# Kernel optimization log

Measured on AMD Instinct MI355X. Metric: run time of the kernel, lower is better.

The kernel has to match this reference:

```python
import jax, jax.numpy as jnp
import numpy as np

N = 50000

def _norm_coeffs(edge_index, n):
    # add self-loops, compute symmetric GCN normalization D^-1/2 (A+I) D^-1/2
    loops = jnp.arange(n, dtype=edge_index.dtype)
    src = jnp.concatenate([edge_index[0], loops])
    dst = jnp.concatenate([edge_index[1], loops])
    deg = jax.ops.segment_sum(jnp.ones_like(dst, dtype=jnp.float32), dst, num_segments=n)
    dinv = jnp.where(deg > 0, jax.lax.rsqrt(deg), 0.0)
    norm = dinv[src] * dinv[dst]  # [E+N]
    return src, dst, norm

def _gcn(x, W, b, src, dst, norm, n):
    h = x @ W                                   # [N, out]
    m = h[src] * norm[:, None]                  # [E+N, out] gather + scale
    return jax.ops.segment_sum(m, dst, num_segments=n) + b

def setup_inputs() -> dict:
    key = jax.random.key(0)
    ks = jax.random.split(key, 8)
    d, h = 96, 96
    E = 800000
    return {
        "x": jax.random.normal(ks[0], (N, d), jnp.float32),
        "edge_index": jax.random.randint(ks[1], (2, E), 0, N, dtype=jnp.int64),
        "h_prev": jax.random.normal(ks[2], (N, h), jnp.float32),
        "Wx": jax.random.normal(ks[3], (d, h), jnp.float32) * (1.0 / np.sqrt(d)),
        "bx": jnp.zeros((h,), jnp.float32),
        "Wuh": jax.random.normal(ks[4], (2 * h, h), jnp.float32) * (1.0 / np.sqrt(2 * h)),
        "buh": jnp.zeros((h,), jnp.float32),
        "Wch": jax.random.normal(ks[5], (2 * h, h), jnp.float32) * (1.0 / np.sqrt(2 * h)),
        "bch": jnp.zeros((h,), jnp.float32),
    }

def reference(x, edge_index, h_prev, Wx, bx, Wuh, buh, Wch, bch):
    n = x.shape[0]
    src, dst, norm = _norm_coeffs(edge_index, n)
    x_gcn = _gcn(x, Wx, bx, src, dst, norm, n)
    combined = jnp.concatenate([x_gcn, h_prev], axis=1)
    # original computes gcn_uh(combined) twice for u and r; identical math -> compute once
    g = jax.nn.sigmoid(_gcn(combined, Wuh, buh, src, dst, norm, n))
    u = g
    r = g
    combined_r = jnp.concatenate([x_gcn, r * h_prev], axis=1)
    c = jnp.tanh(_gcn(combined_r, Wch, bch, src, dst, norm, n))
    return u * h_prev + (1.0 - u) * c
```

## Files before the change

### kernel.cpp

```cpp
#include <hip/hip_runtime.h>
#include <hip/hip_bf16.h>

#define D 96
typedef long long i64;

typedef __bf16 bf16x8 __attribute__((ext_vector_type(8)));
typedef float f32x16 __attribute__((ext_vector_type(16)));

__device__ __forceinline__ float bf2f(unsigned short u) {
  union { unsigned u; float f; } x; x.u = ((unsigned)u) << 16; return x.f;
}
__device__ __forceinline__ void unpack8(uint4 p, float* a) {
  a[0] = bf2f((unsigned short)(p.x & 0xffff)); a[1] = bf2f((unsigned short)(p.x >> 16));
  a[2] = bf2f((unsigned short)(p.y & 0xffff)); a[3] = bf2f((unsigned short)(p.y >> 16));
  a[4] = bf2f((unsigned short)(p.z & 0xffff)); a[5] = bf2f((unsigned short)(p.z >> 16));
  a[6] = bf2f((unsigned short)(p.w & 0xffff)); a[7] = bf2f((unsigned short)(p.w >> 16));
}

__global__ __launch_bounds__(256) void k_zero_detect(int* deg, int N,
                                                     const unsigned* __restrict__ w,
                                                     int* flag, int E) {
  int i = blockIdx.x * 256 + threadIdx.x;
  if (i < N) deg[i] = 0;
  if (blockIdx.x == 0 && threadIdx.x < 64) {
    int lane = threadIdx.x;
    int lim = (E < 2048) ? E : 2048;
    unsigned acc = 0;
    for (int j = lane; j < lim; j += 64) acc |= w[2 * j + 1];
#pragma unroll
    for (int off = 32; off > 0; off >>= 1) acc |= __shfl_down(acc, off, 64);
    if (lane == 0) *flag = (acc == 0) ? 1 : 0;
  }
}

__global__ __launch_bounds__(256) void k_fillpad(const int* __restrict__ e32,
                                                 const i64* __restrict__ e64,
                                                 const int* __restrict__ flagp,
                                                 int* deg, int* __restrict__ csrp,
                                                 int E, int N) {
  int f = *flagp;
  int stride = gridDim.x * 256;
  for (int i = blockIdx.x * 256 + threadIdx.x; i < E; i += stride) {
    int d = f ? (int)e64[(size_t)E + i] : e32[(size_t)E + i];
    if ((unsigned)d >= (unsigned)N) continue;
    int s = f ? (int)e64[i] : e32[i];
    int r = atomicAdd(&deg[d], 1);
    if (r < 128) csrp[((size_t)d << 7) + r] = s;
  }
}

template <int KTOT, int MODE>
__global__ __launch_bounds__(256) void gemm_mfma(
    const float* __restrict__ xin, const float* __restrict__ xg,
    const float* __restrict__ hprev, const float* __restrict__ gmul,
    const float* __restrict__ W, const int* __restrict__ deg,
    __hip_bfloat16* __restrict__ t, int N) {
  __shared__ __align__(16) unsigned short Ah[4][129][8];
  __shared__ __align__(16) unsigned short Al[4][129][8];
  __shared__ __align__(16) unsigned short Wh[4][97][8];
  __shared__ __align__(16) unsigned short Wl[4][97][8];
  const int tid = threadIdx.x;
  const int lane = tid & 63;
  const int wave = tid >> 6;
  const int lr = lane & 31;
  const int kg = lane >> 5;
  const int rb = blockIdx.x * 128;

  f32x16 acc0, acc1, acc2;
#pragma unroll
  for (int i = 0; i < 16; i++) { acc0[i] = 0.f; acc1[i] = 0.f; acc2[i] = 0.f; }

  const int arow = tid >> 3;
  const int ak0 = (tid & 7) * 4;

  for (int kc = 0; kc < KTOT; kc += 32) {
    if (kc) __syncthreads();
#pragma unroll
    for (int p = 0; p < 4; p++) {
      int row = arow + p * 32;
      int grow = rb + row;
      float4 v = make_float4(0.f, 0.f, 0.f, 0.f);
      int gk = kc + ak0;
      if (grow < N) {
        if (MODE == 0) {
          v = *(const float4*)&xin[(size_t)grow * D + gk];
        } else if (gk < 96) {
          v = *(const float4*)&xg[(size_t)grow * D + gk];
        } else {
          v = *(const float4*)&hprev[(size_t)grow * D + (gk - 96)];
          if (MODE == 2) {
            float4 gm = *(const float4*)&gmul[(size_t)grow * D + (gk - 96)];
            v.x *= gm.x; v.y *= gm.y; v.z *= gm.z; v.w *= gm.w;
          }
        }
      }
      unsigned ux = __float_as_uint(v.x), uy = __float_as_uint(v.y);
      unsigned uz = __float_as_uint(v.z), uw = __float_as_uint(v.w);
      unsigned h01 = (uy & 0xffff0000u) | (ux >> 16);
      unsigned h23 = (uw & 0xffff0000u) | (uz >> 16);
      float lx = v.x - __uint_as_float(ux & 0xffff0000u);
      float ly = v.y - __uint_as_float(uy & 0xffff0000u);
      float lz = v.z - __uint_as_float(uz & 0xffff0000u);
      float lw = v.w - __uint_as_float(uw & 0xffff0000u);
      unsigned l01 = (__float_as_uint(ly) & 0xffff0000u) | (__float_as_uint(lx) >> 16);
      unsigned l23 = (__float_as_uint(lw) & 0xffff0000u) | (__float_as_uint(lz) >> 16);
      int kb = ak0 >> 3, ki = ak0 & 7;
      *(uint2*)&Ah[kb][row][ki] = make_uint2(h01, h23);
      *(uint2*)&Al[kb][row][ki] = make_uint2(l01, l23);
    }
#pragma unroll
    for (int p = 0; p < 3; p++) {
      int idx = tid + p * 256;
      int kq = idx / 96;
      int c = idx - kq * 96;
      int k0 = kq * 4;
      const float* wp = &W[(size_t)(kc + k0) * D + c];
      float w0 = wp[0], w1 = wp[D], w2 = wp[2 * D], w3 = wp[3 * D];
      unsigned u0 = __float_as_uint(w0), u1 = __float_as_uint(w1);
      unsigned u2 = __float_as_uint(w2), u3 = __float_as_uint(w3);
      unsigned h01 = (u1 & 0xffff0000u) | (u0 >> 16);
      unsigned h23 = (u3 & 0xffff0000u) | (u2 >> 16);
      float l0 = w0 - __uint_as_float(u0 & 0xffff0000u);
      float l1 = w1 - __uint_as_float(u1 & 0xffff0000u);
      float l2 = w2 - __uint_as_float(u2 & 0xffff0000u);
      float l3 = w3 - __uint_as_float(u3 & 0xffff0000u);
      unsigned l01 = (__float_as_uint(l1) & 0xffff0000u) | (__float_as_uint(l0) >> 16);
      unsigned l23 = (__float_as_uint(l3) & 0xffff0000u) | (__float_as_uint(l2) >> 16);
      int kb = k0 >> 3, ki = k0 & 7;
      *(uint2*)&Wh[kb][c][ki] = make_uint2(h01, h23);
      *(uint2*)&Wl[kb][c][ki] = make_uint2(l01, l23);
    }
    __syncthreads();
#pragma unroll
    for (int s = 0; s < 2; s++) {
      int kb = 2 * s + kg;
      bf16x8 ah = *(const bf16x8*)&Ah[kb][32 * wave + lr][0];
      bf16x8 al = *(const bf16x8*)&Al[kb][32 * wave + lr][0];
      bf16x8 b0h = *(const bf16x8*)&Wh[kb][lr][0];
      bf16x8 b1h = *(const bf16x8*)&Wh[kb][32 + lr][0];
      bf16x8 b2h = *(const bf16x8*)&Wh[kb][64 + lr][0];
      bf16x8 b0l = *(const bf16x8*)&Wl[kb][lr][0];
      bf16x8 b1l = *(const bf16x8*)&Wl[kb][32 + lr][0];
      bf16x8 b2l = *(const bf16x8*)&Wl[kb][64 + lr][0];
      acc0 = __builtin_amdgcn_mfma_f32_32x32x16_bf16(ah, b0h, acc0, 0, 0, 0);
      acc1 = __builtin_amdgcn_mfma_f32_32x32x16_bf16(ah, b1h, acc1, 0, 0, 0);
      acc2 = __builtin_amdgcn_mfma_f32_32x32x16_bf16(ah, b2h, acc2, 0, 0, 0);
      acc0 = __builtin_amdgcn_mfma_f32_32x32x16_bf16(al, b0h, acc0, 0, 0, 0);
      acc1 = __builtin_amdgcn_mfma_f32_32x32x16_bf16(al, b1h, acc1, 0, 0, 0);
      acc2 = __builtin_amdgcn_mfma_f32_32x32x16_bf16(al, b2h, acc2, 0, 0, 0);
      acc0 = __builtin_amdgcn_mfma_f32_32x32x16_bf16(ah, b0l, acc0, 0, 0, 0);
      acc1 = __builtin_amdgcn_mfma_f32_32x32x16_bf16(ah, b1l, acc1, 0, 0, 0);
      acc2 = __builtin_amdgcn_mfma_f32_32x32x16_bf16(ah, b2l, acc2, 0, 0, 0);
    }
  }
  const int rbase = rb + 32 * wave + 4 * kg;
#pragma unroll
  for (int r = 0; r < 16; r++) {
    int row = rbase + (r & 3) + 8 * (r >> 2);
    if (row >= N) continue;
    float dv = rsqrtf((float)deg[row] + 1.0f);
    __hip_bfloat16* tp = &t[(size_t)row * D];
    tp[lr]      = __float2bfloat16(acc0[r] * dv);
    tp[lr + 32] = __float2bfloat16(acc1[r] * dv);
    tp[lr + 64] = __float2bfloat16(acc2[r] * dv);
  }
}

template <int MODE>
__global__ __launch_bounds__(256) void gather_fin(
    const __hip_bfloat16* __restrict__ t, const int* __restrict__ deg,
    const int* __restrict__ csrp,
    const float* __restrict__ bias,
    const float* __restrict__ g, const float* __restrict__ hprev,
    float* __restrict__ outf, int N) {
  int idx = blockIdx.x * 256 + threadIdx.x;
  int total = N * 12;
  if (idx >= total) return;
  int v = idx / 12;
  int c8 = idx - v * 12;
  const uint4* t8 = (const uint4*)t;
  float acc[8];
  unpack8(t8[(size_t)v * 12 + c8], acc);
  int dv_i = deg[v];
  int b0 = v << 7;
  int b1 = b0 + min(dv_i, 128);
  int j = b0;
  for (; j + 8 <= b1; j += 8) {
    int s0 = csrp[j],     s1 = csrp[j + 1], s2 = csrp[j + 2], s3 = csrp[j + 3];
    int s4 = csrp[j + 4], s5 = csrp[j + 5], s6 = csrp[j + 6], s7 = csrp[j + 7];
    uint4 p0 = t8[(size_t)s0 * 12 + c8];
    uint4 p1 = t8[(size_t)s1 * 12 + c8];
    uint4 p2 = t8[(size_t)s2 * 12 + c8];
    uint4 p3 = t8[(size_t)s3 * 12 + c8];
    uint4 p4 = t8[(size_t)s4 * 12 + c8];
    uint4 p5 = t8[(size_t)s5 * 12 + c8];
    uint4 p6 = t8[(size_t)s6 * 12 + c8];
    uint4 p7 = t8[(size_t)s7 * 12 + c8];
    float a0[8], a1[8], a2[8], a3[8], a4[8], a5[8], a6[8], a7[8];
    unpack8(p0, a0); unpack8(p1, a1); unpack8(p2, a2); unpack8(p3, a3);
    unpack8(p4, a4); unpack8(p5, a5); unpack8(p6, a6); unpack8(p7, a7);
#pragma unroll
    for (int q = 0; q < 8; q++)
      acc[q] += ((a0[q] + a1[q]) + (a2[q] + a3[q])) + ((a4[q] + a5[q]) + (a6[q] + a7[q]));
  }
  for (; j + 4 <= b1; j += 4) {
    int s0 = csrp[j], s1 = csrp[j + 1], s2 = csrp[j + 2], s3 = csrp[j + 3];
    uint4 p0 = t8[(size_t)s0 * 12 + c8];
    uint4 p1 = t8[(size_t)s1 * 12 + c8];
    uint4 p2 = t8[(size_t)s2 * 12 + c8];
    uint4 p3 = t8[(size_t)s3 * 12 + c8];
    float a0[8], a1[8], a2[8], a3[8];
    unpack8(p0, a0); unpack8(p1, a1); unpack8(p2, a2); unpack8(p3, a3);
#pragma unroll
    for (int q = 0; q < 8; q++) acc[q] += (a0[q] + a1[q]) + (a2[q] + a3[q]);
  }
  for (; j < b1; j++) {
    int s = csrp[j];
    float a0[8];
    unpack8(t8[(size_t)s * 12 + c8], a0);
#pragma unroll
    for (int q = 0; q < 8; q++) acc[q] += a0[q];
  }
  float dv = rsqrtf((float)dv_i + 1.0f);
  float4 bA = ((const float4*)bias)[c8 * 2];
  float4 bB = ((const float4*)bias)[c8 * 2 + 1];
  float z[8] = {dv * acc[0] + bA.x, dv * acc[1] + bA.y, dv * acc[2] + bA.z, dv * acc[3] + bA.w,
                dv * acc[4] + bB.x, dv * acc[5] + bB.y, dv * acc[6] + bB.z, dv * acc[7] + bB.w};
  float4 oA, oB;
  if (MODE == 1) {
    oA = make_float4(z[0], z[1], z[2], z[3]);
    oB = make_float4(z[4], z[5], z[6], z[7]);
  } else if (MODE == 2) {
    oA = make_float4(1.0f / (1.0f + expf(-z[0])), 1.0f / (1.0f + expf(-z[1])),
                     1.0f / (1.0f + expf(-z[2])), 1.0f / (1.0f + expf(-z[3])));
    oB = make_float4(1.0f / (1.0f + expf(-z[4])), 1.0f / (1.0f + expf(-z[5])),
                     1.0f / (1.0f + expf(-z[6])), 1.0f / (1.0f + expf(-z[7])));
  } else {
    float4 uA = ((const float4*)g)[idx * 2], uB = ((const float4*)g)[idx * 2 + 1];
    float4 hA = ((const float4*)hprev)[idx * 2], hB = ((const float4*)hprev)[idx * 2 + 1];
    oA = make_float4(uA.x * hA.x + (1.0f - uA.x) * tanhf(z[0]),
                     uA.y * hA.y + (1.0f - uA.y) * tanhf(z[1]),
                     uA.z * hA.z + (1.0f - uA.z) * tanhf(z[2]),
                     uA.w * hA.w + (1.0f - uA.w) * tanhf(z[3]));
    oB = make_float4(uB.x * hB.x + (1.0f - uB.x) * tanhf(z[4]),
                     uB.y * hB.y + (1.0f - uB.y) * tanhf(z[5]),
                     uB.z * hB.z + (1.0f - uB.z) * tanhf(z[6]),
                     uB.w * hB.w + (1.0f - uB.w) * tanhf(z[7]));
  }
  ((float4*)outf)[idx * 2] = oA;
  ((float4*)outf)[idx * 2 + 1] = oB;
}

extern "C" void kernel_launch(void* const* d_in, const int* in_sizes, int n_in,
                              void* d_out, int out_size, void* d_ws, size_t ws_size,
                              hipStream_t stream) {
  const float* x = (const float*)d_in[0];
  const int* ei32 = (const int*)d_in[1];
  const i64* ei64 = (const i64*)d_in[1];
  const unsigned* eiw = (const unsigned*)d_in[1];
  const float* hp = (const float*)d_in[2];
  const float* Wx = (const float*)d_in[3];
  const float* bx = (const float*)d_in[4];
  const float* Wuh = (const float*)d_in[5];
  const float* buh = (const float*)d_in[6];
  const float* Wch = (const float*)d_in[7];
  const float* bch = (const float*)d_in[8];
  float* out = (float*)d_out;

  const int N = in_sizes[0] / D;
  const int E = in_sizes[1] / 2;
  const size_t NF = (size_t)N * D;
  const size_t nPad = ((size_t)N + 1023) & ~(size_t)1023;

  char* base = (char*)d_ws;
  int* flag = (int*)base;
  int* deg = (int*)(base + 256);
  int* csrp = deg + nPad;
  __hip_bfloat16* t = (__hip_bfloat16*)(csrp + nPad * 128);
  float* xg = (float*)((char*)t + NF * 2);
  float* g = xg + NF;

  const int nbN = (N + 255) / 256;
  const int gb = (N + 127) / 128;
  const int fb8 = (N * 12 + 255) / 256;
  const int pb = 2048;

  k_zero_detect<<<nbN, 256, 0, stream>>>(deg, N, eiw, flag, E);
  k_fillpad<<<pb, 256, 0, stream>>>(ei32, ei64, flag, deg, csrp, E, N);

  gemm_mfma<96, 0><<<gb, 256, 0, stream>>>(x, nullptr, nullptr, nullptr, Wx, deg, t, N);
  gather_fin<1><<<fb8, 256, 0, stream>>>(t, deg, csrp, bx, nullptr, nullptr, xg, N);

  gemm_mfma<192, 1><<<gb, 256, 0, stream>>>(nullptr, xg, hp, nullptr, Wuh, deg, t, N);
  gather_fin<2><<<fb8, 256, 0, stream>>>(t, deg, csrp, buh, nullptr, nullptr, g, N);

  gemm_mfma<192, 2><<<gb, 256, 0, stream>>>(nullptr, xg, hp, g, Wch, deg, t, N);
  gather_fin<3><<<fb8, 256, 0, stream>>>(t, deg, csrp, bch, g, hp, out, N);
}
```

Measured before the change: 302.4 us.

## Build padded CSR via two-pass shared-memory bucketing instead of global atomics

Replaces the global-atomic padded-CSR fill with a two-pass scheme. Each of 256 blocks buckets its edge chunk by destination group (dst>>8) using shared-memory atomics into a region matrix. A second kernel per group then assembles a 256-node CSR slab in LDS and writes it out coalesced. The per-node cap drops from 128 to 64, which halves the CSR footprint. The goal is to cut random global atomic contention and scattered writes. The risks are silently dropping edges when a per-(group,block) cell exceeds 64, or when a node's in-degree exceeds 64. k_csr also uses 64KB of LDS per block, which limits occupancy.

```diff
diff --git a/kernel.cpp b/kernel.cpp
--- a/kernel.cpp
+++ b/kernel.cpp
@@ -2,6 +2,7 @@
 #include <hip/hip_bf16.h>
 
 #define D 96
+#define CAP 64
 typedef long long i64;
 
 typedef __bf16 bf16x8 __attribute__((ext_vector_type(8)));
@@ -17,12 +18,9 @@
   a[6] = bf2f((unsigned short)(p.w & 0xffff)); a[7] = bf2f((unsigned short)(p.w >> 16));
 }
 
-__global__ __launch_bounds__(256) void k_zero_detect(int* deg, int N,
-                                                     const unsigned* __restrict__ w,
-                                                     int* flag, int E) {
-  int i = blockIdx.x * 256 + threadIdx.x;
-  if (i < N) deg[i] = 0;
-  if (blockIdx.x == 0 && threadIdx.x < 64) {
+__global__ __launch_bounds__(256) void k_detect(const unsigned* __restrict__ w,
+                                                int* flag, int E) {
+  if (threadIdx.x < 64) {
     int lane = threadIdx.x;
     int lim = (E < 2048) ? E : 2048;
     unsigned acc = 0;
@@ -33,20 +31,60 @@
   }
 }
 
-__global__ __launch_bounds__(256) void k_fillpad(const int* __restrict__ e32,
-                                                 const i64* __restrict__ e64,
-                                                 const int* __restrict__ flagp,
-                                                 int* deg, int* __restrict__ csrp,
-                                                 int E, int N) {
-  int f = *flagp;
-  int stride = gridDim.x * 256;
-  for (int i = blockIdx.x * 256 + threadIdx.x; i < E; i += stride) {
-    int d = f ? (int)e64[(size_t)E + i] : e32[(size_t)E + i];
-    if ((unsigned)d >= (unsigned)N) continue;
-    int s = f ? (int)e64[i] : e32[i];
-    int r = atomicAdd(&deg[d], 1);
-    if (r < 128) csrp[((size_t)d << 7) + r] = s;
-  }
+__global__ __launch_bounds__(256) void k_bucket(const int* __restrict__ e32,
+                                                const i64* __restrict__ e64,
+                                                const int* __restrict__ flagp,
+                                                uint2* __restrict__ region,
+                                                int* __restrict__ cntmat,
+                                                int E, int N, int NB) {
+  __shared__ int lofs[256];
+  const int tid = threadIdx.x;
+  const int blk = blockIdx.x;
+  lofs[tid] = 0;
+  __syncthreads();
+  const int f = *flagp;
+  const int chunk = (E + gridDim.x - 1) / gridDim.x;
+  const int lo = blk * chunk;
+  const int hi = min(E, lo + chunk);
+  for (int i = lo + tid; i < hi; i += 256) {
+    int d, s;
+    if (f) { d = (int)e64[(size_t)E + i]; s = (int)e64[i]; }
+    else   { d = e32[(size_t)E + i];      s = e32[i]; }
+    if ((unsigned)d >= (unsigned)N || (unsigned)s >= (unsigned)N) continue;
+    int q = d >> 8;
+    int r = atomicAdd(&lofs[q], 1);
+    if (r < CAP)
+      region[((size_t)q * 256 + blk) * CAP + r] = make_uint2((unsigned)s, (unsigned)d);
+  }
+  __syncthreads();
+  if (tid < NB) cntmat[blk * 256 + tid] = min(lofs[tid], CAP);
+}
+
+__global__ __launch_bounds__(256) void k_csr(const uint2* __restrict__ region,
+                                             const int* __restrict__ cntmat,
+                                             int* __restrict__ deg,
+                                             int* __restrict__ csrp, int NB) {
+  __shared__ int ldeg[256];
+  __shared__ int lcsr[256 * CAP];
+  const int tid = threadIdx.x;
+  const int b = blockIdx.x;
+  ldeg[tid] = 0;
+  __syncthreads();
+  int cnt = cntmat[tid * 256 + b];
+  const uint2* cell = region + ((size_t)b * 256 + tid) * CAP;
+  for (int k = 0; k < cnt; k++) {
+    uint2 e = cell[k];
+    int node = (int)(e.y & 255u);
+    int r = atomicAdd(&ldeg[node], 1);
+    if (r < CAP) lcsr[node * CAP + r] = (int)e.x;
+  }
+  __syncthreads();
+  deg[(b << 8) + tid] = ldeg[tid];
+  const uint4* src = (const uint4*)lcsr;
+  uint4* dst = (uint4*)(csrp + ((size_t)b << 8) * CAP);
+#pragma unroll
+  for (int it = 0; it < (256 * CAP) / 4 / 256; it++)
+    dst[tid + it * 256] = src[tid + it * 256];
 }
 
 template <int KTOT, int MODE>
@@ -182,8 +220,8 @@
   float acc[8];
   unpack8(t8[(size_t)v * 12 + c8], acc);
   int dv_i = deg[v];
-  int b0 = v << 7;
-  int b1 = b0 + min(dv_i, 128);
+  int b0 = v * CAP;
+  int b1 = b0 + min(dv_i, CAP);
   int j = b0;
   for (; j + 8 <= b1; j += 8) {
     int s0 = csrp[j],     s1 = csrp[j + 1], s2 = csrp[j + 2], s3 = csrp[j + 3];
@@ -270,23 +308,25 @@
   const int N = in_sizes[0] / D;
   const int E = in_sizes[1] / 2;
   const size_t NF = (size_t)N * D;
-  const size_t nPad = ((size_t)N + 1023) & ~(size_t)1023;
+  const int NB = (N + 255) >> 8;
+  const int R = NB << 8;
 
   char* base = (char*)d_ws;
   int* flag = (int*)base;
   int* deg = (int*)(base + 256);
-  int* csrp = deg + nPad;
-  __hip_bfloat16* t = (__hip_bfloat16*)(csrp + nPad * 128);
+  int* cntmat = deg + R;
+  uint2* region = (uint2*)(cntmat + 65536);
+  int* csrp = (int*)(region + (size_t)NB * 256 * CAP);
+  __hip_bfloat16* t = (__hip_bfloat16*)(csrp + (size_t)R * CAP);
   float* xg = (float*)((char*)t + NF * 2);
   float* g = xg + NF;
 
-  const int nbN = (N + 255) / 256;
   const int gb = (N + 127) / 128;
   const int fb8 = (N * 12 + 255) / 256;
-  const int pb = 2048;
-
-  k_zero_detect<<<nbN, 256, 0, stream>>>(deg, N, eiw, flag, E);
-  k_fillpad<<<pb, 256, 0, stream>>>(ei32, ei64, flag, deg, csrp, E, N);
+
+  k_detect<<<1, 256, 0, stream>>>(eiw, flag, E);
+  k_bucket<<<256, 256, 0, stream>>>(ei32, ei64, flag, region, cntmat, E, N, NB);
+  k_csr<<<NB, 256, 0, stream>>>(region, cntmat, deg, csrp, NB);
 
   gemm_mfma<96, 0><<<gb, 256, 0, stream>>>(x, nullptr, nullptr, nullptr, Wx, deg, t, N);
   gather_fin<1><<<fb8, 256, 0, stream>>>(t, deg, csrp, bx, nullptr, nullptr, xg, N);
```

New measurement: 265.8 us. 12.1% less time.
